# Kernel optimization log

Hardware: AMD Instinct MI355X
Metric: run time of the kernel (lower is better)

Reference implementation:

```python
import jax, jax.numpy as jnp
import numpy as np

B, S, D = 1, 2048, 2048
HQ, HKV, DH = 16, 4, 128
WINDOW = 512  # sliding window encoded in explicit attn_mask


def rotate_half(u):
    u1, u2 = jnp.split(u, 2, axis=-1)
    return jnp.concatenate([-u2, u1], axis=-1)


def setup_inputs() -> dict:
    key = jax.random.key(0)
    ks = jax.random.split(key, 6)
    x = jax.random.normal(ks[0], (B, S, D), dtype=jnp.float32)
    # RoPE caches (standard rotary frequencies, full d_head with duplicated halves)
    pos = jnp.arange(S)
    inv_freq = 1.0 / (10000.0 ** (jnp.arange(0, DH, 2, dtype=jnp.float32) / DH))
    ang = pos[:, None].astype(jnp.float32) * inv_freq[None, :]  # [S, DH/2]
    emb = jnp.concatenate([ang, ang], axis=-1)                  # [S, DH]
    cos_cache = jnp.cos(emb)
    sin_cache = jnp.sin(emb)
    # sliding-window causal mask: attend to j<=i and i-j < WINDOW
    i = jnp.arange(S)[:, None]
    j = jnp.arange(S)[None, :]
    attn_mask = (j <= i) & ((i - j) < WINDOW)
    sc = 0.02
    Wq = jax.random.normal(ks[1], (D, HQ * DH), dtype=jnp.float32) * sc
    Wk = jax.random.normal(ks[2], (D, HKV * DH), dtype=jnp.float32) * sc
    Wv = jax.random.normal(ks[3], (D, HKV * DH), dtype=jnp.float32) * sc
    Wo = jax.random.normal(ks[4], (HQ * DH, D), dtype=jnp.float32) * sc
    return {"x": x, "cos_cache": cos_cache, "sin_cache": sin_cache,
            "positions": pos.astype(jnp.int64), "attn_mask": attn_mask,
            "Wq": Wq, "Wk": Wk, "Wv": Wv, "Wo": Wo}


def reference(x, cos_cache, sin_cache, positions, attn_mask, Wq, Wk, Wv, Wo):
    batch, seq_len, _ = x.shape
    Q = (x @ Wq).reshape(batch, seq_len, HQ, DH).transpose(0, 2, 1, 3)   # [B,HQ,S,DH]
    K = (x @ Wk).reshape(batch, seq_len, HKV, DH).transpose(0, 2, 1, 3)  # [B,HKV,S,DH]
    V = (x @ Wv).reshape(batch, seq_len, HKV, DH).transpose(0, 2, 1, 3)
    # RoPE
    cos = cos_cache[positions][None, None, :, :]  # [1,1,S,DH]
    sin = sin_cache[positions][None, None, :, :]
    Q = Q * cos + rotate_half(Q) * sin
    K = K * cos + rotate_half(K) * sin
    # GQA expansion (repeat_interleave along head dim)
    G = HQ // HKV
    K_exp = jnp.repeat(K, G, axis=1)  # [B,HQ,S,DH]
    V_exp = jnp.repeat(V, G, axis=1)
    scores = jnp.einsum('bhqd,bhkd->bhqk', Q, K_exp) / jnp.sqrt(jnp.float32(DH))
    neg_inf = jnp.finfo(scores.dtype).min
    scores = jnp.where(attn_mask[None, None, :, :], scores, neg_inf)
    weights = jax.nn.softmax(scores, axis=-1)
    attn_out = jnp.einsum('bhqk,bhkd->bhqd', weights, V_exp)
    attn_out = attn_out.transpose(0, 2, 1, 3).reshape(batch, seq_len, HQ * DH)
    output = attn_out @ Wo
    return (output, K, V)  # new kv cache is the (post-RoPE) K, V
```

## Files before the change

### kernel.cpp

```cpp
#include <hip/hip_runtime.h>
#include <stdint.h>

typedef unsigned short u16;
typedef __attribute__((ext_vector_type(4))) float f32x4;
typedef __attribute__((ext_vector_type(8))) short short8;
typedef __attribute__((ext_vector_type(4))) short short4v;

__device__ inline u16 f2bf(float f) {
  union { float f; uint32_t u; } v; v.f = f;
  uint32_t u = v.u;
  u += 0x7fffu + ((u >> 16) & 1u);
  return (u16)(u >> 16);
}
__device__ inline float bf2f(u16 b) {
  union { uint32_t u; float f; } v; v.u = (uint32_t)b << 16; return v.f;
}

__global__ __launch_bounds__(256) void k_prep(const float* __restrict__ x,
                                              const float* __restrict__ Wq, const float* __restrict__ Wk,
                                              const float* __restrict__ Wv, const float* __restrict__ Wo,
                                              u16* __restrict__ xb, u16* __restrict__ WT, u16* __restrict__ WoT) {
  const int b = blockIdx.x, tid = threadIdx.x;
  if (b < 1024) {
    size_t base = (size_t)b * 4096 + tid * 4;
    #pragma unroll
    for (int k = 0; k < 4; ++k) {
      f32x4 v = *(const f32x4*)(x + base + k * 1024);
      short4v o;
      o.x = (short)f2bf(v.x); o.y = (short)f2bf(v.y);
      o.z = (short)f2bf(v.z); o.w = (short)f2bf(v.w);
      *(short4v*)(xb + base + k * 1024) = o;
    }
    return;
  }
  __shared__ float t[64][68];
  const float* W; u16* D; int N, bb;
  if (b < 2048)      { W = Wq; D = WT;                       N = 2048; bb = b - 1024; }
  else if (b < 2304) { W = Wk; D = WT + (size_t)2048 * 2048; N = 512;  bb = b - 2048; }
  else if (b < 2560) { W = Wv; D = WT + (size_t)2560 * 2048; N = 512;  bb = b - 2304; }
  else               { W = Wo; D = WoT;                      N = 2048; bb = b - 2560; }
  const int nb = N >> 6;
  const int n0 = (bb % nb) * 64, k0 = (bb / nb) * 64;
  const int c4 = (tid & 15) * 4, rbase = tid >> 4;
  #pragma unroll
  for (int p = 0; p < 4; ++p) {
    int r = p * 16 + rbase;
    *(f32x4*)&t[r][c4] = *(const f32x4*)&W[(size_t)(k0 + r) * N + n0 + c4];
  }
  __syncthreads();
  const int i = tid >> 2, j = (tid & 3) * 16;
  short8 o0, o1;
  #pragma unroll
  for (int m = 0; m < 8; ++m) o0[m] = (short)f2bf(t[j + m][i]);
  #pragma unroll
  for (int m = 0; m < 8; ++m) o1[m] = (short)f2bf(t[j + 8 + m][i]);
  *(short8*)&D[(size_t)(n0 + i) * 2048 + k0 + j] = o0;
  *(short8*)&D[(size_t)(n0 + i) * 2048 + k0 + j + 8] = o1;
}

__global__ __launch_bounds__(512, 2) void k_gemmqkv(const u16* __restrict__ A,
                                                    const u16* __restrict__ B,
                                                    u16* __restrict__ C) {
  const int K = 2048;
  const int NT = 32;
  __shared__ __align__(16) u16 lds[3 * 20480];
  const int tid = threadIdx.x;
  const int wid = tid >> 6, lane = tid & 63;
  const int quad = lane >> 4, l16 = lane & 15;
  const int wm = (wid >> 2) * 64;
  const int wn = (wid & 3) * 48;
  const int bm = blockIdx.y * 128, bn = blockIdx.x * 192;

  const u16* aSrc[2]; int aDst[2];
  #pragma unroll
  for (int L = 0; L < 2; ++L) {
    int E = (tid + L * 512) * 8;
    int r = E >> 6, pc = (E >> 3) & 7;
    int lc = pc ^ (r & 7);
    aSrc[L] = A + (size_t)(bm + r) * K + lc * 8;
    aDst[L] = E;
  }
  const u16* bSrc[3]; int bDst[3];
  #pragma unroll
  for (int L = 0; L < 3; ++L) {
    int E = (tid + L * 512) * 8;
    int r = E >> 6, pc = (E >> 3) & 7;
    int lc = pc ^ (r & 7);
    bSrc[L] = B + (size_t)(bn + r) * K + lc * 8;
    bDst[L] = 8192 + E;
  }

  #define STAGE(buf, kt) do {                                                              \
    _Pragma("unroll")                                                                      \
    for (int L = 0; L < 2; ++L)                                                            \
      __builtin_amdgcn_global_load_lds(                                                    \
          (const __attribute__((address_space(1))) void*)(aSrc[L] + (kt) * 64),            \
          (__attribute__((address_space(3))) void*)(&lds[(buf) * 20480 + aDst[L]]), 16, 0, 0); \
    _Pragma("unroll")                                                                      \
    for (int L = 0; L < 3; ++L)                                                            \
      __builtin_amdgcn_global_load_lds(                                                    \
          (const __attribute__((address_space(1))) void*)(bSrc[L] + (kt) * 64),            \
          (__attribute__((address_space(3))) void*)(&lds[(buf) * 20480 + bDst[L]]), 16, 0, 0); \
  } while (0)

  f32x4 acc[4][3];
  #pragma unroll
  for (int m = 0; m < 4; ++m)
    #pragma unroll
    for (int n = 0; n < 3; ++n) acc[m][n] = (f32x4){0.f, 0.f, 0.f, 0.f};

  STAGE(0, 0);
  STAGE(1, 1);
  asm volatile("s_waitcnt vmcnt(5)" ::: "memory");
  __builtin_amdgcn_s_barrier();

  int c = 0, p = 2;
  for (int t = 0; t < NT; ++t) {
    if (t + 2 < NT) STAGE(p, t + 2);

    short8 af[4][2], bf[3][2];
    #pragma unroll
    for (int mf = 0; mf < 4; ++mf)
      #pragma unroll
      for (int kc = 0; kc < 2; ++kc) {
        int R = wm + mf * 16 + l16;
        int pc = (kc * 4 + quad) ^ (R & 7);
        af[mf][kc] = *(const short8*)&lds[c * 20480 + R * 64 + pc * 8];
      }
    #pragma unroll
    for (int nf = 0; nf < 3; ++nf)
      #pragma unroll
      for (int kc = 0; kc < 2; ++kc) {
        int Cc = wn + nf * 16 + l16;
        int pc = (kc * 4 + quad) ^ (Cc & 7);
        bf[nf][kc] = *(const short8*)&lds[c * 20480 + 8192 + Cc * 64 + pc * 8];
      }

    __builtin_amdgcn_s_setprio(1);
    #pragma unroll
    for (int mf = 0; mf < 4; ++mf)
      #pragma unroll
      for (int nf = 0; nf < 3; ++nf)
        #pragma unroll
        for (int kc = 0; kc < 2; ++kc)
          acc[mf][nf] = __builtin_amdgcn_mfma_f32_16x16x32_bf16(af[mf][kc], bf[nf][kc], acc[mf][nf], 0, 0, 0);
    __builtin_amdgcn_s_setprio(0);

    if (t + 2 < NT) {
      asm volatile("s_waitcnt vmcnt(5)" ::: "memory");
    } else if (t + 1 < NT) {
      asm volatile("s_waitcnt vmcnt(0)" ::: "memory");
    }
    __builtin_amdgcn_s_barrier();
    c = (c == 2) ? 0 : c + 1;
    p = (p == 2) ? 0 : p + 1;
  }
  #undef STAGE

  #pragma unroll
  for (int mf = 0; mf < 4; ++mf) {
    int row = bm + wm + mf * 16 + quad * 4;
    #pragma unroll
    for (int nf = 0; nf < 3; ++nf) {
      int col = bn + wn + nf * 16 + l16;
      #pragma unroll
      for (int r = 0; r < 4; ++r)
        C[(size_t)(row + r) * 3072 + col] = f2bf(acc[mf][nf][r]);
    }
  }
}

__global__ __launch_bounds__(512, 2) void k_gemmo(const u16* __restrict__ A,
                                                  const u16* __restrict__ B,
                                                  float* __restrict__ C) {
  const int K = 2048;
  const int NT = 32;
  __shared__ __align__(16) u16 lds[3 * 16384];
  const int tid = threadIdx.x;
  const int wid = tid >> 6, lane = tid & 63;
  const int quad = lane >> 4, l16 = lane & 15;
  const int wm = (wid >> 2) * 64;
  const int wn = (wid & 3) * 32;
  const int bm = blockIdx.y * 128, bn = blockIdx.x * 128;

  const u16* aSrc[2]; const u16* bSrc[2]; int dDst[2];
  #pragma unroll
  for (int L = 0; L < 2; ++L) {
    int E = (tid + L * 512) * 8;
    int r = E >> 6, pc = (E >> 3) & 7;
    int lc = pc ^ (r & 7);
    aSrc[L] = A + (size_t)(bm + r) * K + lc * 8;
    bSrc[L] = B + (size_t)(bn + r) * K + lc * 8;
    dDst[L] = E;
  }

  #define STAGEO(buf, kt) do {                                                             \
    _Pragma("unroll")                                                                      \
    for (int L = 0; L < 2; ++L)                                                            \
      __builtin_amdgcn_global_load_lds(                                                    \
          (const __attribute__((address_space(1))) void*)(aSrc[L] + (kt) * 64),            \
          (__attribute__((address_space(3))) void*)(&lds[(buf) * 16384 + dDst[L]]), 16, 0, 0); \
    _Pragma("unroll")                                                                      \
    for (int L = 0; L < 2; ++L)                                                            \
      __builtin_amdgcn_global_load_lds(                                                    \
          (const __attribute__((address_space(1))) void*)(bSrc[L] + (kt) * 64),            \
          (__attribute__((address_space(3))) void*)(&lds[(buf) * 16384 + 8192 + dDst[L]]), 16, 0, 0); \
  } while (0)

  f32x4 acc[4][2];
  #pragma unroll
  for (int m = 0; m < 4; ++m)
    #pragma unroll
    for (int n = 0; n < 2; ++n) acc[m][n] = (f32x4){0.f, 0.f, 0.f, 0.f};

  STAGEO(0, 0);
  STAGEO(1, 1);
  asm volatile("s_waitcnt vmcnt(4)" ::: "memory");
  __builtin_amdgcn_s_barrier();

  int c = 0, p = 2;
  for (int t = 0; t < NT; ++t) {
    if (t + 2 < NT) STAGEO(p, t + 2);

    short8 af[4][2], bf[2][2];
    #pragma unroll
    for (int mf = 0; mf < 4; ++mf)
      #pragma unroll
      for (int kc = 0; kc < 2; ++kc) {
        int R = wm + mf * 16 + l16;
        int pc = (kc * 4 + quad) ^ (R & 7);
        af[mf][kc] = *(const short8*)&lds[c * 16384 + R * 64 + pc * 8];
      }
    #pragma unroll
    for (int nf = 0; nf < 2; ++nf)
      #pragma unroll
      for (int kc = 0; kc < 2; ++kc) {
        int Cc = wn + nf * 16 + l16;
        int pc = (kc * 4 + quad) ^ (Cc & 7);
        bf[nf][kc] = *(const short8*)&lds[c * 16384 + 8192 + Cc * 64 + pc * 8];
      }

    __builtin_amdgcn_s_setprio(1);
    #pragma unroll
    for (int mf = 0; mf < 4; ++mf)
      #pragma unroll
      for (int nf = 0; nf < 2; ++nf)
        #pragma unroll
        for (int kc = 0; kc < 2; ++kc)
          acc[mf][nf] = __builtin_amdgcn_mfma_f32_16x16x32_bf16(af[mf][kc], bf[nf][kc], acc[mf][nf], 0, 0, 0);
    __builtin_amdgcn_s_setprio(0);

    if (t + 2 < NT) {
      asm volatile("s_waitcnt vmcnt(4)" ::: "memory");
    } else if (t + 1 < NT) {
      asm volatile("s_waitcnt vmcnt(0)" ::: "memory");
    }
    __builtin_amdgcn_s_barrier();
    c = (c == 2) ? 0 : c + 1;
    p = (p == 2) ? 0 : p + 1;
  }
  #undef STAGEO

  #pragma unroll
  for (int mf = 0; mf < 4; ++mf) {
    int row = bm + wm + mf * 16 + quad * 4;
    #pragma unroll
    for (int nf = 0; nf < 2; ++nf) {
      int col = bn + wn + nf * 16 + l16;
      #pragma unroll
      for (int r = 0; r < 4; ++r)
        C[(size_t)(row + r) * 2048 + col] = acc[mf][nf][r];
    }
  }
}

__global__ __launch_bounds__(256) void k_post(const u16* __restrict__ P,
                                              const float* __restrict__ cosc, const float* __restrict__ sinc,
                                              u16* __restrict__ Qb, u16* __restrict__ Kb, u16* __restrict__ Vt,
                                              float* __restrict__ Kout, float* __restrict__ Vout) {
  const int b = blockIdx.x, tid = threadIdx.x;
  if (b < 2048) {
    __shared__ float row[3072];
    const int s = b;
    const u16* p0 = P + (size_t)s * 3072;
    for (int i = tid * 4; i < 3072; i += 1024) {
      short4v a0 = *(const short4v*)(p0 + i);
      #pragma unroll
      for (int m = 0; m < 4; ++m)
        row[i + m] = bf2f((u16)a0[m]);
    }
    __syncthreads();
    const int d = tid & 127;
    const int hbase = tid >> 7;
    const float c = cosc[s * 128 + d], sn = sinc[s * 128 + d];
    const float scale = 0.08838834764831845f;
    #pragma unroll
    for (int it = 0; it < 12; ++it) {
      int slice = it * 2 + hbase;
      float v = row[slice * 128 + d];
      if (slice < 20) {
        float other = (d < 64) ? -row[slice * 128 + d + 64] : row[slice * 128 + d - 64];
        float r = v * c + other * sn;
        if (slice < 16) {
          Qb[((size_t)slice * 2048 + s) * 128 + d] = f2bf(r * scale);
        } else {
          int hk = slice - 16;
          Kout[((size_t)hk * 2048 + s) * 128 + d] = r;
          Kb[((size_t)hk * 2048 + s) * 128 + d] = f2bf(r);
        }
      } else {
        int hv = slice - 20;
        Vout[((size_t)hv * 2048 + s) * 128 + d] = v;
      }
    }
  } else {
    __shared__ float t[32][33];
    const int b2 = b - 2048;
    const int c0 = (b2 & 15) * 32, s0 = (b2 >> 4) * 32;
    const int tx = tid & 31, ty = tid >> 5;
    #pragma unroll
    for (int i = ty; i < 32; i += 8) {
      size_t idx = (size_t)(s0 + i) * 3072 + 2560 + c0 + tx;
      t[i][tx] = bf2f(P[idx]);
    }
    __syncthreads();
    const int head = c0 >> 7, dbase = c0 & 127;
    #pragma unroll
    for (int i = ty; i < 32; i += 8)
      Vt[((size_t)head * 128 + dbase + i) * 2048 + s0 + tx] = f2bf(t[tx][i]);
  }
}

__global__ __launch_bounds__(512) void k_attn(const u16* __restrict__ Qb,
                                              const u16* __restrict__ Kb,
                                              const u16* __restrict__ Vt,
                                              u16* __restrict__ O) {
  const int qt = blockIdx.x;
  const int hk = blockIdx.y;
  const int tid = threadIdx.x;
  const int wid = tid >> 6, lane = tid & 63;
  const int quad = lane >> 4, l16 = lane & 15;
  const int h = hk * 4 + (wid >> 1);
  const int qrow0 = qt * 32;
  const int r0 = qrow0 + (wid & 1) * 16;
  const u16* Qh = Qb + (size_t)h * 2048 * 128;
  const u16* Kh = Kb + (size_t)hk * 2048 * 128;
  const u16* Vh = Vt + (size_t)hk * 128 * 2048;

  __shared__ u16 Ks[3][32 * 136];
  __shared__ u16 Vs[3][128 * 40];
  __shared__ u16 Ps[8][16 * 40];

  short8 qa[4];
  #pragma unroll
  for (int ks = 0; ks < 4; ++ks)
    qa[ks] = *(const short8*)&Qh[(size_t)(r0 + l16) * 128 + ks * 32 + quad * 8];

  f32x4 o[8];
  #pragma unroll
  for (int dt = 0; dt < 8; ++dt) o[dt] = (f32x4){0.f, 0.f, 0.f, 0.f};
  float lsum[4] = {0.f, 0.f, 0.f, 0.f};

  const int c0 = qrow0 > 511 ? (qrow0 - 511) >> 5 : 0;
  const int c1 = (qrow0 + 31) >> 5;

  const int krow = tid >> 4, kcol = (tid & 15) * 8;
  const int vrow = tid >> 2, vcol = (tid & 3) * 8;

  short8 kreg, vreg;
  {
    const int jb = c0 * 32;
    kreg = *(const short8*)&Kh[(size_t)(jb + krow) * 128 + kcol];
    vreg = *(const short8*)&Vh[(size_t)vrow * 2048 + jb + vcol];
  }

  for (int c = c0; c <= c1; ++c) {
    const int b = c % 3;
    const int jbase = c * 32;
    *(short8*)&Ks[b][krow * 136 + kcol] = kreg;
    *(short8*)&Vs[b][vrow * 40 + vcol] = vreg;
    if (c < c1) {
      const int jb = jbase + 32;
      kreg = *(const short8*)&Kh[(size_t)(jb + krow) * 128 + kcol];
      vreg = *(const short8*)&Vh[(size_t)vrow * 2048 + jb + vcol];
    }
    __syncthreads();

    f32x4 sc[2];
    #pragma unroll
    for (int ni = 0; ni < 2; ++ni) {
      sc[ni] = (f32x4){0.f, 0.f, 0.f, 0.f};
      #pragma unroll
      for (int ks = 0; ks < 4; ++ks) {
        short8 kf = *(const short8*)&Ks[b][(ni * 16 + l16) * 136 + ks * 32 + quad * 8];
        sc[ni] = __builtin_amdgcn_mfma_f32_16x16x32_bf16(qa[ks], kf, sc[ni], 0, 0, 0);
      }
    }
    #pragma unroll
    for (int ni = 0; ni < 2; ++ni) {
      const int jlo = jbase + ni * 16;
      const bool none = (jlo > r0 + 15) || (jlo + 15 < r0 - 511);
      const bool allv = (jlo + 15 <= r0) && (jlo >= r0 - 496);
      float p[4];
      if (none) {
        p[0] = p[1] = p[2] = p[3] = 0.f;
      } else if (allv) {
        #pragma unroll
        for (int r = 0; r < 4; ++r) p[r] = __expf(sc[ni][r]);
      } else {
        const int j = jlo + l16;
        #pragma unroll
        for (int r = 0; r < 4; ++r) {
          int i = r0 + quad * 4 + r;
          bool ok = (j <= i) && (i - j < 512);
          p[r] = ok ? __expf(sc[ni][r]) : 0.f;
        }
      }
      #pragma unroll
      for (int r = 0; r < 4; ++r) {
        lsum[r] += p[r];
        Ps[wid][(quad * 4 + r) * 40 + ni * 16 + l16] = f2bf(p[r]);
      }
    }
    short8 pa = *(const short8*)&Ps[wid][l16 * 40 + quad * 8];
    #pragma unroll
    for (int dt = 0; dt < 8; ++dt) {
      short8 vf = *(const short8*)&Vs[b][(dt * 16 + l16) * 40 + quad * 8];
      o[dt] = __builtin_amdgcn_mfma_f32_16x16x32_bf16(pa, vf, o[dt], 0, 0, 0);
    }
  }

  #pragma unroll
  for (int off = 1; off < 16; off <<= 1)
    #pragma unroll
    for (int r = 0; r < 4; ++r)
      lsum[r] += __shfl_xor(lsum[r], off, 64);
  float inv[4];
  #pragma unroll
  for (int r = 0; r < 4; ++r) inv[r] = 1.0f / lsum[r];

  #pragma unroll
  for (int dt = 0; dt < 8; ++dt) {
    int col = h * 128 + dt * 16 + l16;
    #pragma unroll
    for (int r = 0; r < 4; ++r) {
      int row = r0 + quad * 4 + r;
      O[(size_t)row * 2048 + col] = f2bf(o[dt][r] * inv[r]);
    }
  }
}

extern "C" void kernel_launch(void* const* d_in, const int* in_sizes, int n_in,
                              void* d_out, int out_size, void* d_ws, size_t ws_size,
                              hipStream_t stream) {
  const float* x    = (const float*)d_in[0];
  const float* cosc = (const float*)d_in[1];
  const float* sinc = (const float*)d_in[2];
  const float* Wq = (const float*)d_in[5];
  const float* Wk = (const float*)d_in[6];
  const float* Wv = (const float*)d_in[7];
  const float* Wo = (const float*)d_in[8];

  char* ws = (char*)d_ws;
  u16*   xb    = (u16*)(ws);
  u16*   O     = (u16*)(ws);
  u16*   WT    = (u16*)(ws + (8u  << 20));
  u16*   WoT   = (u16*)(ws + (20u << 20));
  u16*   Qb    = (u16*)(ws + (28u << 20));
  u16*   Kb    = (u16*)(ws + (36u << 20));
  u16*   Vt    = (u16*)(ws + (38u << 20));
  u16*   QKV   = (u16*)(ws + (40u << 20));

  float* outO = (float*)d_out;
  float* outK = (float*)d_out + 4194304;
  float* outV = (float*)d_out + 5242880;

  k_prep<<<3584, 256, 0, stream>>>(x, Wq, Wk, Wv, Wo, xb, WT, WoT);
  k_gemmqkv<<<dim3(16, 16), 512, 0, stream>>>(xb, WT, QKV);
  k_post<<<3072, 256, 0, stream>>>(QKV, cosc, sinc, Qb, Kb, Vt, outK, outV);
  k_attn<<<dim3(64, 4), 512, 0, stream>>>(Qb, Kb, Vt, O);
  k_gemmo<<<dim3(16, 16), 512, 0, stream>>>(O, WoT, outO);
}
```

Measured before the change: 101.6 us.

## Fuse RoPE and Q/K scatter into QKV GEMM epilogue via permuted weight columns

The weight-prep kernel now permutes Wq/Wk output columns so each rotate-half pair (d, d+64) sits in adjacent columns. The QKV GEMM epilogue can then apply RoPE with a lane shuffle and write Qb, Kb and the fp32 K output directly. The post kernel shrinks to a V-only transpose that also writes the fp32 V output. This removes the full bf16 QKV round trip through global memory and most of the post kernel. The cost is scattered, uncoalesced epilogue stores plus per-element cos/sin loads inside the GEMM. It also relies on the permuted Q/K head-dim layout in Qb/Kb being harmless, which holds only because attention takes a dot product over the head dimension.

Result: slower. 107.5 us (+5.8%).

```diff
diff --git a/kernel.cpp b/kernel.cpp
--- a/kernel.cpp
+++ b/kernel.cpp
@@ -34,33 +34,45 @@
     return;
   }
   __shared__ float t[64][68];
-  const float* W; u16* D; int N, bb;
-  if (b < 2048)      { W = Wq; D = WT;                       N = 2048; bb = b - 1024; }
-  else if (b < 2304) { W = Wk; D = WT + (size_t)2048 * 2048; N = 512;  bb = b - 2048; }
-  else if (b < 2560) { W = Wv; D = WT + (size_t)2560 * 2048; N = 512;  bb = b - 2304; }
-  else               { W = Wo; D = WoT;                      N = 2048; bb = b - 2560; }
+  const float* W; u16* D; int N, bb; bool perm;
+  if (b < 2048)      { W = Wq; D = WT;                       N = 2048; bb = b - 1024; perm = true;  }
+  else if (b < 2304) { W = Wk; D = WT + (size_t)2048 * 2048; N = 512;  bb = b - 2048; perm = true;  }
+  else if (b < 2560) { W = Wv; D = WT + (size_t)2560 * 2048; N = 512;  bb = b - 2304; perm = false; }
+  else               { W = Wo; D = WoT;                      N = 2048; bb = b - 2560; perm = false; }
   const int nb = N >> 6;
   const int n0 = (bb % nb) * 64, k0 = (bb / nb) * 64;
   const int c4 = (tid & 15) * 4, rbase = tid >> 4;
+  int scol;
+  if (perm) {
+    int S0 = (n0 & ~127) + ((n0 >> 6) & 1) * 32;
+    scol = (c4 < 32) ? (S0 + c4) : (S0 + 64 + (c4 - 32));
+  } else {
+    scol = n0 + c4;
+  }
   #pragma unroll
   for (int p = 0; p < 4; ++p) {
     int r = p * 16 + rbase;
-    *(f32x4*)&t[r][c4] = *(const f32x4*)&W[(size_t)(k0 + r) * N + n0 + c4];
+    *(f32x4*)&t[r][c4] = *(const f32x4*)&W[(size_t)(k0 + r) * N + scol];
   }
   __syncthreads();
   const int i = tid >> 2, j = (tid & 3) * 16;
+  const int tcol = perm ? ((i >> 1) + 32 * (i & 1)) : i;
   short8 o0, o1;
   #pragma unroll
-  for (int m = 0; m < 8; ++m) o0[m] = (short)f2bf(t[j + m][i]);
-  #pragma unroll
-  for (int m = 0; m < 8; ++m) o1[m] = (short)f2bf(t[j + 8 + m][i]);
+  for (int m = 0; m < 8; ++m) o0[m] = (short)f2bf(t[j + m][tcol]);
+  #pragma unroll
+  for (int m = 0; m < 8; ++m) o1[m] = (short)f2bf(t[j + 8 + m][tcol]);
   *(short8*)&D[(size_t)(n0 + i) * 2048 + k0 + j] = o0;
   *(short8*)&D[(size_t)(n0 + i) * 2048 + k0 + j + 8] = o1;
 }
 
 __global__ __launch_bounds__(512, 2) void k_gemmqkv(const u16* __restrict__ A,
                                                     const u16* __restrict__ B,
-                                                    u16* __restrict__ C) {
+                                                    const float* __restrict__ cosc,
+                                                    const float* __restrict__ sinc,
+                                                    u16* __restrict__ Qb, u16* __restrict__ Kb,
+                                                    float* __restrict__ Kout,
+                                                    u16* __restrict__ Vraw) {
   const int K = 2048;
   const int NT = 32;
   __shared__ __align__(16) u16 lds[3 * 20480];
@@ -157,15 +169,39 @@
   }
   #undef STAGE
 
+  const float scale = 0.08838834764831845f;
   #pragma unroll
   for (int mf = 0; mf < 4; ++mf) {
-    int row = bm + wm + mf * 16 + quad * 4;
+    int srow = bm + wm + mf * 16 + quad * 4;
     #pragma unroll
     for (int nf = 0; nf < 3; ++nf) {
-      int col = bn + wn + nf * 16 + l16;
-      #pragma unroll
-      for (int r = 0; r < 4; ++r)
-        C[(size_t)(row + r) * 3072 + col] = f2bf(acc[mf][nf][r]);
+      int cb = bn + wn + nf * 16;
+      if (cb >= 2560) {
+        #pragma unroll
+        for (int r = 0; r < 4; ++r)
+          Vraw[(size_t)(srow + r) * 512 + (cb - 2560) + l16] = f2bf(acc[mf][nf][r]);
+      } else {
+        const int tcol = (cb & 127) + l16;
+        const int pp = tcol >> 1;
+        const int odd = l16 & 1;
+        #pragma unroll
+        for (int r = 0; r < 4; ++r) {
+          float v = acc[mf][nf][r];
+          float w = __shfl_xor(v, 1, 64);
+          int s = srow + r;
+          float cc = cosc[s * 128 + pp];
+          float ss = sinc[s * 128 + pp];
+          float res = odd ? (v * cc + w * ss) : (v * cc - w * ss);
+          if (cb < 2048) {
+            int h = cb >> 7;
+            Qb[((size_t)h * 2048 + s) * 128 + tcol] = f2bf(res * scale);
+          } else {
+            int hk = (cb - 2048) >> 7;
+            Kb[((size_t)hk * 2048 + s) * 128 + tcol] = f2bf(res);
+            Kout[((size_t)hk * 2048 + s) * 128 + pp + 64 * odd] = res;
+          }
+        }
+      }
     }
   }
 }
@@ -274,60 +310,22 @@
   }
 }
 
-__global__ __launch_bounds__(256) void k_post(const u16* __restrict__ P,
-                                              const float* __restrict__ cosc, const float* __restrict__ sinc,
-                                              u16* __restrict__ Qb, u16* __restrict__ Kb, u16* __restrict__ Vt,
-                                              float* __restrict__ Kout, float* __restrict__ Vout) {
-  const int b = blockIdx.x, tid = threadIdx.x;
-  if (b < 2048) {
-    __shared__ float row[3072];
-    const int s = b;
-    const u16* p0 = P + (size_t)s * 3072;
-    for (int i = tid * 4; i < 3072; i += 1024) {
-      short4v a0 = *(const short4v*)(p0 + i);
-      #pragma unroll
-      for (int m = 0; m < 4; ++m)
-        row[i + m] = bf2f((u16)a0[m]);
-    }
-    __syncthreads();
-    const int d = tid & 127;
-    const int hbase = tid >> 7;
-    const float c = cosc[s * 128 + d], sn = sinc[s * 128 + d];
-    const float scale = 0.08838834764831845f;
-    #pragma unroll
-    for (int it = 0; it < 12; ++it) {
-      int slice = it * 2 + hbase;
-      float v = row[slice * 128 + d];
-      if (slice < 20) {
-        float other = (d < 64) ? -row[slice * 128 + d + 64] : row[slice * 128 + d - 64];
-        float r = v * c + other * sn;
-        if (slice < 16) {
-          Qb[((size_t)slice * 2048 + s) * 128 + d] = f2bf(r * scale);
-        } else {
-          int hk = slice - 16;
-          Kout[((size_t)hk * 2048 + s) * 128 + d] = r;
-          Kb[((size_t)hk * 2048 + s) * 128 + d] = f2bf(r);
-        }
-      } else {
-        int hv = slice - 20;
-        Vout[((size_t)hv * 2048 + s) * 128 + d] = v;
-      }
-    }
-  } else {
-    __shared__ float t[32][33];
-    const int b2 = b - 2048;
-    const int c0 = (b2 & 15) * 32, s0 = (b2 >> 4) * 32;
-    const int tx = tid & 31, ty = tid >> 5;
-    #pragma unroll
-    for (int i = ty; i < 32; i += 8) {
-      size_t idx = (size_t)(s0 + i) * 3072 + 2560 + c0 + tx;
-      t[i][tx] = bf2f(P[idx]);
-    }
-    __syncthreads();
-    const int head = c0 >> 7, dbase = c0 & 127;
-    #pragma unroll
-    for (int i = ty; i < 32; i += 8)
-      Vt[((size_t)head * 128 + dbase + i) * 2048 + s0 + tx] = f2bf(t[tx][i]);
+__global__ __launch_bounds__(256) void k_post(const u16* __restrict__ Vraw,
+                                              u16* __restrict__ Vt, float* __restrict__ Vout) {
+  __shared__ float t[32][33];
+  const int b2 = blockIdx.x;
+  const int c0 = (b2 & 15) * 32, s0 = (b2 >> 4) * 32;
+  const int tid = threadIdx.x;
+  const int tx = tid & 31, ty = tid >> 5;
+  #pragma unroll
+  for (int i = ty; i < 32; i += 8)
+    t[i][tx] = bf2f(Vraw[(size_t)(s0 + i) * 512 + c0 + tx]);
+  __syncthreads();
+  const int head = c0 >> 7, dbase = c0 & 127;
+  #pragma unroll
+  for (int i = ty; i < 32; i += 8) {
+    Vt[((size_t)head * 128 + dbase + i) * 2048 + s0 + tx] = f2bf(t[tx][i]);
+    Vout[((size_t)head * 2048 + s0 + i) * 128 + dbase + tx] = t[i][tx];
   }
 }
 
@@ -469,15 +467,15 @@
   u16*   Qb    = (u16*)(ws + (28u << 20));
   u16*   Kb    = (u16*)(ws + (36u << 20));
   u16*   Vt    = (u16*)(ws + (38u << 20));
-  u16*   QKV   = (u16*)(ws + (40u << 20));
+  u16*   Vraw  = (u16*)(ws + (40u << 20));
 
   float* outO = (float*)d_out;
   float* outK = (float*)d_out + 4194304;
   float* outV = (float*)d_out + 5242880;
 
   k_prep<<<3584, 256, 0, stream>>>(x, Wq, Wk, Wv, Wo, xb, WT, WoT);
-  k_gemmqkv<<<dim3(16, 16), 512, 0, stream>>>(xb, WT, QKV);
-  k_post<<<3072, 256, 0, stream>>>(QKV, cosc, sinc, Qb, Kb, Vt, outK, outV);
+  k_gemmqkv<<<dim3(16, 16), 512, 0, stream>>>(xb, WT, cosc, sinc, Qb, Kb, outK, Vraw);
+  k_post<<<1024, 256, 0, stream>>>(Vraw, Vt, outV);
   k_attn<<<dim3(64, 4), 512, 0, stream>>>(Qb, Kb, Vt, O);
   k_gemmo<<<dim3(16, 16), 512, 0, stream>>>(O, WoT, outO);
 }
```

## Double GEMM block threads to 1024 and split A/B tile loading across waves

Applied to the files above, without the earlier changes.

Both projection GEMMs now launch 1024-thread blocks (16 waves), with each wave computing a 32-row slice instead of 64 rows of the same 128-row block tile. Global-to-LDS staging is split so the first 512 threads load the A tile and the rest load the B tile, and the per-thread vmcnt waits are adjusted to match. The intent is more waves per CU to hide memory and MFMA latency while keeping the grid unchanged. The cost is that each fragment read from LDS is reused across fewer MFMAs, and the launch-bounds setting tightens register limits.

Measured after the change: 104.0 us. 1.02x slower.

```diff
diff --git a/kernel.cpp b/kernel.cpp
--- a/kernel.cpp
+++ b/kernel.cpp
@@ -58,69 +58,65 @@
   *(short8*)&D[(size_t)(n0 + i) * 2048 + k0 + j + 8] = o1;
 }
 
-__global__ __launch_bounds__(512, 2) void k_gemmqkv(const u16* __restrict__ A,
-                                                    const u16* __restrict__ B,
-                                                    u16* __restrict__ C) {
+__global__ __launch_bounds__(1024, 4) void k_gemmqkv(const u16* __restrict__ A,
+                                                     const u16* __restrict__ B,
+                                                     u16* __restrict__ C) {
   const int K = 2048;
   const int NT = 32;
   __shared__ __align__(16) u16 lds[3 * 20480];
   const int tid = threadIdx.x;
   const int wid = tid >> 6, lane = tid & 63;
   const int quad = lane >> 4, l16 = lane & 15;
-  const int wm = (wid >> 2) * 64;
+  const int wm = (wid >> 2) * 32;
   const int wn = (wid & 3) * 48;
   const int bm = blockIdx.y * 128, bn = blockIdx.x * 192;
 
-  const u16* aSrc[2]; int aDst[2];
-  #pragma unroll
-  for (int L = 0; L < 2; ++L) {
-    int E = (tid + L * 512) * 8;
+  const bool isA = tid < 512;
+  const int ts = isA ? tid : tid - 512;
+  const u16* src[3]; int dst[3];
+  #pragma unroll
+  for (int L = 0; L < 3; ++L) {
+    int s = ts + L * 512;
+    if (isA && L == 2) s = ts;
+    int E = s * 8;
     int r = E >> 6, pc = (E >> 3) & 7;
     int lc = pc ^ (r & 7);
-    aSrc[L] = A + (size_t)(bm + r) * K + lc * 8;
-    aDst[L] = E;
-  }
-  const u16* bSrc[3]; int bDst[3];
-  #pragma unroll
-  for (int L = 0; L < 3; ++L) {
-    int E = (tid + L * 512) * 8;
-    int r = E >> 6, pc = (E >> 3) & 7;
-    int lc = pc ^ (r & 7);
-    bSrc[L] = B + (size_t)(bn + r) * K + lc * 8;
-    bDst[L] = 8192 + E;
+    if (isA) { src[L] = A + (size_t)(bm + r) * K + lc * 8; dst[L] = E; }
+    else     { src[L] = B + (size_t)(bn + r) * K + lc * 8; dst[L] = 8192 + E; }
   }
 
   #define STAGE(buf, kt) do {                                                              \
-    _Pragma("unroll")                                                                      \
-    for (int L = 0; L < 2; ++L)                                                            \
+    __builtin_amdgcn_global_load_lds(                                                      \
+        (const __attribute__((address_space(1))) void*)(src[0] + (kt) * 64),               \
+        (__attribute__((address_space(3))) void*)(&lds[(buf) * 20480 + dst[0]]), 16, 0, 0);\
+    __builtin_amdgcn_global_load_lds(                                                      \
+        (const __attribute__((address_space(1))) void*)(src[1] + (kt) * 64),               \
+        (__attribute__((address_space(3))) void*)(&lds[(buf) * 20480 + dst[1]]), 16, 0, 0);\
+    if (!isA)                                                                              \
       __builtin_amdgcn_global_load_lds(                                                    \
-          (const __attribute__((address_space(1))) void*)(aSrc[L] + (kt) * 64),            \
-          (__attribute__((address_space(3))) void*)(&lds[(buf) * 20480 + aDst[L]]), 16, 0, 0); \
-    _Pragma("unroll")                                                                      \
-    for (int L = 0; L < 3; ++L)                                                            \
-      __builtin_amdgcn_global_load_lds(                                                    \
-          (const __attribute__((address_space(1))) void*)(bSrc[L] + (kt) * 64),            \
-          (__attribute__((address_space(3))) void*)(&lds[(buf) * 20480 + bDst[L]]), 16, 0, 0); \
+          (const __attribute__((address_space(1))) void*)(src[2] + (kt) * 64),             \
+          (__attribute__((address_space(3))) void*)(&lds[(buf) * 20480 + dst[2]]), 16, 0, 0);\
   } while (0)
 
-  f32x4 acc[4][3];
-  #pragma unroll
-  for (int m = 0; m < 4; ++m)
+  f32x4 acc[2][3];
+  #pragma unroll
+  for (int m = 0; m < 2; ++m)
     #pragma unroll
     for (int n = 0; n < 3; ++n) acc[m][n] = (f32x4){0.f, 0.f, 0.f, 0.f};
 
   STAGE(0, 0);
   STAGE(1, 1);
-  asm volatile("s_waitcnt vmcnt(5)" ::: "memory");
+  if (isA) { asm volatile("s_waitcnt vmcnt(2)" ::: "memory"); }
+  else     { asm volatile("s_waitcnt vmcnt(3)" ::: "memory"); }
   __builtin_amdgcn_s_barrier();
 
   int c = 0, p = 2;
   for (int t = 0; t < NT; ++t) {
     if (t + 2 < NT) STAGE(p, t + 2);
 
-    short8 af[4][2], bf[3][2];
-    #pragma unroll
-    for (int mf = 0; mf < 4; ++mf)
+    short8 af[2][2], bf[3][2];
+    #pragma unroll
+    for (int mf = 0; mf < 2; ++mf)
       #pragma unroll
       for (int kc = 0; kc < 2; ++kc) {
         int R = wm + mf * 16 + l16;
@@ -138,7 +134,7 @@
 
     __builtin_amdgcn_s_setprio(1);
     #pragma unroll
-    for (int mf = 0; mf < 4; ++mf)
+    for (int mf = 0; mf < 2; ++mf)
       #pragma unroll
       for (int nf = 0; nf < 3; ++nf)
         #pragma unroll
@@ -147,7 +143,8 @@
     __builtin_amdgcn_s_setprio(0);
 
     if (t + 2 < NT) {
-      asm volatile("s_waitcnt vmcnt(5)" ::: "memory");
+      if (isA) { asm volatile("s_waitcnt vmcnt(2)" ::: "memory"); }
+      else     { asm volatile("s_waitcnt vmcnt(3)" ::: "memory"); }
     } else if (t + 1 < NT) {
       asm volatile("s_waitcnt vmcnt(0)" ::: "memory");
     }
@@ -158,7 +155,7 @@
   #undef STAGE
 
   #pragma unroll
-  for (int mf = 0; mf < 4; ++mf) {
+  for (int mf = 0; mf < 2; ++mf) {
     int row = bm + wm + mf * 16 + quad * 4;
     #pragma unroll
     for (int nf = 0; nf < 3; ++nf) {
@@ -170,61 +167,57 @@
   }
 }
 
-__global__ __launch_bounds__(512, 2) void k_gemmo(const u16* __restrict__ A,
-                                                  const u16* __restrict__ B,
-                                                  float* __restrict__ C) {
+__global__ __launch_bounds__(1024, 4) void k_gemmo(const u16* __restrict__ A,
+                                                   const u16* __restrict__ B,
+                                                   float* __restrict__ C) {
   const int K = 2048;
   const int NT = 32;
   __shared__ __align__(16) u16 lds[3 * 16384];
   const int tid = threadIdx.x;
   const int wid = tid >> 6, lane = tid & 63;
   const int quad = lane >> 4, l16 = lane & 15;
-  const int wm = (wid >> 2) * 64;
+  const int wm = (wid >> 2) * 32;
   const int wn = (wid & 3) * 32;
   const int bm = blockIdx.y * 128, bn = blockIdx.x * 128;
 
-  const u16* aSrc[2]; const u16* bSrc[2]; int dDst[2];
+  const bool isA = tid < 512;
+  const int ts = isA ? tid : tid - 512;
+  const u16* src[2]; int dst[2];
   #pragma unroll
   for (int L = 0; L < 2; ++L) {
-    int E = (tid + L * 512) * 8;
+    int E = (ts + L * 512) * 8;
     int r = E >> 6, pc = (E >> 3) & 7;
     int lc = pc ^ (r & 7);
-    aSrc[L] = A + (size_t)(bm + r) * K + lc * 8;
-    bSrc[L] = B + (size_t)(bn + r) * K + lc * 8;
-    dDst[L] = E;
+    if (isA) { src[L] = A + (size_t)(bm + r) * K + lc * 8; dst[L] = E; }
+    else     { src[L] = B + (size_t)(bn + r) * K + lc * 8; dst[L] = 8192 + E; }
   }
 
   #define STAGEO(buf, kt) do {                                                             \
     _Pragma("unroll")                                                                      \
     for (int L = 0; L < 2; ++L)                                                            \
       __builtin_amdgcn_global_load_lds(                                                    \
-          (const __attribute__((address_space(1))) void*)(aSrc[L] + (kt) * 64),            \
-          (__attribute__((address_space(3))) void*)(&lds[(buf) * 16384 + dDst[L]]), 16, 0, 0); \
-    _Pragma("unroll")                                                                      \
-    for (int L = 0; L < 2; ++L)                                                            \
-      __builtin_amdgcn_global_load_lds(                                                    \
-          (const __attribute__((address_space(1))) void*)(bSrc[L] + (kt) * 64),            \
-          (__attribute__((address_space(3))) void*)(&lds[(buf) * 16384 + 8192 + dDst[L]]), 16, 0, 0); \
+          (const __attribute__((address_space(1))) void*)(src[L] + (kt) * 64),             \
+          (__attribute__((address_space(3))) void*)(&lds[(buf) * 16384 + dst[L]]), 16, 0, 0); \
   } while (0)
 
-  f32x4 acc[4][2];
-  #pragma unroll
-  for (int m = 0; m < 4; ++m)
+  f32x4 acc[2][2];
+  #pragma unroll
+  for (int m = 0; m < 2; ++m)
     #pragma unroll
     for (int n = 0; n < 2; ++n) acc[m][n] = (f32x4){0.f, 0.f, 0.f, 0.f};
 
   STAGEO(0, 0);
   STAGEO(1, 1);
-  asm volatile("s_waitcnt vmcnt(4)" ::: "memory");
+  asm volatile("s_waitcnt vmcnt(2)" ::: "memory");
   __builtin_amdgcn_s_barrier();
 
   int c = 0, p = 2;
   for (int t = 0; t < NT; ++t) {
     if (t + 2 < NT) STAGEO(p, t + 2);
 
-    short8 af[4][2], bf[2][2];
-    #pragma unroll
-    for (int mf = 0; mf < 4; ++mf)
+    short8 af[2][2], bf[2][2];
+    #pragma unroll
+    for (int mf = 0; mf < 2; ++mf)
       #pragma unroll
       for (int kc = 0; kc < 2; ++kc) {
         int R = wm + mf * 16 + l16;
@@ -242,7 +235,7 @@
 
     __builtin_amdgcn_s_setprio(1);
     #pragma unroll
-    for (int mf = 0; mf < 4; ++mf)
+    for (int mf = 0; mf < 2; ++mf)
       #pragma unroll
       for (int nf = 0; nf < 2; ++nf)
         #pragma unroll
@@ -251,7 +244,7 @@
     __builtin_amdgcn_s_setprio(0);
 
     if (t + 2 < NT) {
-      asm volatile("s_waitcnt vmcnt(4)" ::: "memory");
+      asm volatile("s_waitcnt vmcnt(2)" ::: "memory");
     } else if (t + 1 < NT) {
       asm volatile("s_waitcnt vmcnt(0)" ::: "memory");
     }
@@ -262,7 +255,7 @@
   #undef STAGEO
 
   #pragma unroll
-  for (int mf = 0; mf < 4; ++mf) {
+  for (int mf = 0; mf < 2; ++mf) {
     int row = bm + wm + mf * 16 + quad * 4;
     #pragma unroll
     for (int nf = 0; nf < 2; ++nf) {
@@ -476,8 +469,8 @@
   float* outV = (float*)d_out + 5242880;
 
   k_prep<<<3584, 256, 0, stream>>>(x, Wq, Wk, Wv, Wo, xb, WT, WoT);
-  k_gemmqkv<<<dim3(16, 16), 512, 0, stream>>>(xb, WT, QKV);
+  k_gemmqkv<<<dim3(16, 16), 1024, 0, stream>>>(xb, WT, QKV);
   k_post<<<3072, 256, 0, stream>>>(QKV, cosc, sinc, Qb, Kb, Vt, outK, outV);
   k_attn<<<dim3(64, 4), 512, 0, stream>>>(Qb, Kb, Vt, O);
-  k_gemmo<<<dim3(16, 16), 512, 0, stream>>>(O, WoT, outO);
-}
+  k_gemmo<<<dim3(16, 16), 1024, 0, stream>>>(O, WoT, outO);
+}
```

## Use smaller 256-thread GEMM tiles with simple double buffering

Applied to the files above, without the earlier changes.

Both GEMM kernels move from 512-thread blocks with 128x192/128x128 tiles and a 3-stage async pipeline to 256-thread blocks with 128x96/128x64 tiles and a 2-stage double buffer synchronized by __syncthreads. The grids double to 512 blocks, aiming for better CU coverage and balance. In exchange, per-block data reuse drops and global-load latency is less hidden, since each barrier waits for all outstanding loads. The setprio hints are also removed.

Result: slower. 106.2 us (+4.5%).

```diff
diff --git a/kernel.cpp b/kernel.cpp
--- a/kernel.cpp
+++ b/kernel.cpp
@@ -58,23 +58,23 @@
   *(short8*)&D[(size_t)(n0 + i) * 2048 + k0 + j + 8] = o1;
 }
 
-__global__ __launch_bounds__(512, 2) void k_gemmqkv(const u16* __restrict__ A,
-                                                    const u16* __restrict__ B,
-                                                    u16* __restrict__ C) {
+__global__ __launch_bounds__(256) void k_gemmqkv(const u16* __restrict__ A,
+                                                 const u16* __restrict__ B,
+                                                 u16* __restrict__ C) {
   const int K = 2048;
   const int NT = 32;
-  __shared__ __align__(16) u16 lds[3 * 20480];
+  __shared__ __align__(16) u16 lds[2 * 14336];
   const int tid = threadIdx.x;
   const int wid = tid >> 6, lane = tid & 63;
   const int quad = lane >> 4, l16 = lane & 15;
-  const int wm = (wid >> 2) * 64;
-  const int wn = (wid & 3) * 48;
-  const int bm = blockIdx.y * 128, bn = blockIdx.x * 192;
-
-  const u16* aSrc[2]; int aDst[2];
-  #pragma unroll
-  for (int L = 0; L < 2; ++L) {
-    int E = (tid + L * 512) * 8;
+  const int wm = (wid >> 1) * 64;
+  const int wn = (wid & 1) * 48;
+  const int bm = blockIdx.y * 128, bn = blockIdx.x * 96;
+
+  const u16* aSrc[4]; int aDst[4];
+  #pragma unroll
+  for (int L = 0; L < 4; ++L) {
+    int E = (tid + L * 256) * 8;
     int r = E >> 6, pc = (E >> 3) & 7;
     int lc = pc ^ (r & 7);
     aSrc[L] = A + (size_t)(bm + r) * K + lc * 8;
@@ -83,7 +83,7 @@
   const u16* bSrc[3]; int bDst[3];
   #pragma unroll
   for (int L = 0; L < 3; ++L) {
-    int E = (tid + L * 512) * 8;
+    int E = (tid + L * 256) * 8;
     int r = E >> 6, pc = (E >> 3) & 7;
     int lc = pc ^ (r & 7);
     bSrc[L] = B + (size_t)(bn + r) * K + lc * 8;
@@ -92,15 +92,15 @@
 
   #define STAGE(buf, kt) do {                                                              \
     _Pragma("unroll")                                                                      \
-    for (int L = 0; L < 2; ++L)                                                            \
+    for (int L = 0; L < 4; ++L)                                                            \
       __builtin_amdgcn_global_load_lds(                                                    \
           (const __attribute__((address_space(1))) void*)(aSrc[L] + (kt) * 64),            \
-          (__attribute__((address_space(3))) void*)(&lds[(buf) * 20480 + aDst[L]]), 16, 0, 0); \
+          (__attribute__((address_space(3))) void*)(&lds[(buf) * 14336 + aDst[L]]), 16, 0, 0); \
     _Pragma("unroll")                                                                      \
     for (int L = 0; L < 3; ++L)                                                            \
       __builtin_amdgcn_global_load_lds(                                                    \
           (const __attribute__((address_space(1))) void*)(bSrc[L] + (kt) * 64),            \
-          (__attribute__((address_space(3))) void*)(&lds[(buf) * 20480 + bDst[L]]), 16, 0, 0); \
+          (__attribute__((address_space(3))) void*)(&lds[(buf) * 14336 + bDst[L]]), 16, 0, 0); \
   } while (0)
 
   f32x4 acc[4][3];
@@ -110,13 +110,11 @@
     for (int n = 0; n < 3; ++n) acc[m][n] = (f32x4){0.f, 0.f, 0.f, 0.f};
 
   STAGE(0, 0);
-  STAGE(1, 1);
-  asm volatile("s_waitcnt vmcnt(5)" ::: "memory");
-  __builtin_amdgcn_s_barrier();
-
-  int c = 0, p = 2;
+  __syncthreads();
+
   for (int t = 0; t < NT; ++t) {
-    if (t + 2 < NT) STAGE(p, t + 2);
+    const int c = t & 1;
+    if (t + 1 < NT) STAGE(c ^ 1, t + 1);
 
     short8 af[4][2], bf[3][2];
     #pragma unroll
@@ -125,7 +123,7 @@
       for (int kc = 0; kc < 2; ++kc) {
         int R = wm + mf * 16 + l16;
         int pc = (kc * 4 + quad) ^ (R & 7);
-        af[mf][kc] = *(const short8*)&lds[c * 20480 + R * 64 + pc * 8];
+        af[mf][kc] = *(const short8*)&lds[c * 14336 + R * 64 + pc * 8];
       }
     #pragma unroll
     for (int nf = 0; nf < 3; ++nf)
@@ -133,10 +131,9 @@
       for (int kc = 0; kc < 2; ++kc) {
         int Cc = wn + nf * 16 + l16;
         int pc = (kc * 4 + quad) ^ (Cc & 7);
-        bf[nf][kc] = *(const short8*)&lds[c * 20480 + 8192 + Cc * 64 + pc * 8];
-      }
-
-    __builtin_amdgcn_s_setprio(1);
+        bf[nf][kc] = *(const short8*)&lds[c * 14336 + 8192 + Cc * 64 + pc * 8];
+      }
+
     #pragma unroll
     for (int mf = 0; mf < 4; ++mf)
       #pragma unroll
@@ -144,16 +141,8 @@
         #pragma unroll
         for (int kc = 0; kc < 2; ++kc)
           acc[mf][nf] = __builtin_amdgcn_mfma_f32_16x16x32_bf16(af[mf][kc], bf[nf][kc], acc[mf][nf], 0, 0, 0);
-    __builtin_amdgcn_s_setprio(0);
-
-    if (t + 2 < NT) {
-      asm volatile("s_waitcnt vmcnt(5)" ::: "memory");
-    } else if (t + 1 < NT) {
-      asm volatile("s_waitcnt vmcnt(0)" ::: "memory");
-    }
-    __builtin_amdgcn_s_barrier();
-    c = (c == 2) ? 0 : c + 1;
-    p = (p == 2) ? 0 : p + 1;
+
+    __syncthreads();
   }
   #undef STAGE
 
@@ -170,41 +159,49 @@
   }
 }
 
-__global__ __launch_bounds__(512, 2) void k_gemmo(const u16* __restrict__ A,
-                                                  const u16* __restrict__ B,
-                                                  float* __restrict__ C) {
+__global__ __launch_bounds__(256) void k_gemmo(const u16* __restrict__ A,
+                                               const u16* __restrict__ B,
+                                               float* __restrict__ C) {
   const int K = 2048;
   const int NT = 32;
-  __shared__ __align__(16) u16 lds[3 * 16384];
+  __shared__ __align__(16) u16 lds[2 * 12288];
   const int tid = threadIdx.x;
   const int wid = tid >> 6, lane = tid & 63;
   const int quad = lane >> 4, l16 = lane & 15;
-  const int wm = (wid >> 2) * 64;
-  const int wn = (wid & 3) * 32;
-  const int bm = blockIdx.y * 128, bn = blockIdx.x * 128;
-
-  const u16* aSrc[2]; const u16* bSrc[2]; int dDst[2];
-  #pragma unroll
-  for (int L = 0; L < 2; ++L) {
-    int E = (tid + L * 512) * 8;
+  const int wm = (wid >> 1) * 64;
+  const int wn = (wid & 1) * 32;
+  const int bm = blockIdx.y * 128, bn = blockIdx.x * 64;
+
+  const u16* aSrc[4]; int aDst[4];
+  #pragma unroll
+  for (int L = 0; L < 4; ++L) {
+    int E = (tid + L * 256) * 8;
     int r = E >> 6, pc = (E >> 3) & 7;
     int lc = pc ^ (r & 7);
     aSrc[L] = A + (size_t)(bm + r) * K + lc * 8;
+    aDst[L] = E;
+  }
+  const u16* bSrc[2]; int bDst[2];
+  #pragma unroll
+  for (int L = 0; L < 2; ++L) {
+    int E = (tid + L * 256) * 8;
+    int r = E >> 6, pc = (E >> 3) & 7;
+    int lc = pc ^ (r & 7);
     bSrc[L] = B + (size_t)(bn + r) * K + lc * 8;
-    dDst[L] = E;
+    bDst[L] = 8192 + E;
   }
 
   #define STAGEO(buf, kt) do {                                                             \
     _Pragma("unroll")                                                                      \
-    for (int L = 0; L < 2; ++L)                                                            \
+    for (int L = 0; L < 4; ++L)                                                            \
       __builtin_amdgcn_global_load_lds(                                                    \
           (const __attribute__((address_space(1))) void*)(aSrc[L] + (kt) * 64),            \
-          (__attribute__((address_space(3))) void*)(&lds[(buf) * 16384 + dDst[L]]), 16, 0, 0); \
+          (__attribute__((address_space(3))) void*)(&lds[(buf) * 12288 + aDst[L]]), 16, 0, 0); \
     _Pragma("unroll")                                                                      \
     for (int L = 0; L < 2; ++L)                                                            \
       __builtin_amdgcn_global_load_lds(                                                    \
           (const __attribute__((address_space(1))) void*)(bSrc[L] + (kt) * 64),            \
-          (__attribute__((address_space(3))) void*)(&lds[(buf) * 16384 + 8192 + dDst[L]]), 16, 0, 0); \
+          (__attribute__((address_space(3))) void*)(&lds[(buf) * 12288 + bDst[L]]), 16, 0, 0); \
   } while (0)
 
   f32x4 acc[4][2];
@@ -214,13 +211,11 @@
     for (int n = 0; n < 2; ++n) acc[m][n] = (f32x4){0.f, 0.f, 0.f, 0.f};
 
   STAGEO(0, 0);
-  STAGEO(1, 1);
-  asm volatile("s_waitcnt vmcnt(4)" ::: "memory");
-  __builtin_amdgcn_s_barrier();
-
-  int c = 0, p = 2;
+  __syncthreads();
+
   for (int t = 0; t < NT; ++t) {
-    if (t + 2 < NT) STAGEO(p, t + 2);
+    const int c = t & 1;
+    if (t + 1 < NT) STAGEO(c ^ 1, t + 1);
 
     short8 af[4][2], bf[2][2];
     #pragma unroll
@@ -229,7 +224,7 @@
       for (int kc = 0; kc < 2; ++kc) {
         int R = wm + mf * 16 + l16;
         int pc = (kc * 4 + quad) ^ (R & 7);
-        af[mf][kc] = *(const short8*)&lds[c * 16384 + R * 64 + pc * 8];
+        af[mf][kc] = *(const short8*)&lds[c * 12288 + R * 64 + pc * 8];
       }
     #pragma unroll
     for (int nf = 0; nf < 2; ++nf)
@@ -237,10 +232,9 @@
       for (int kc = 0; kc < 2; ++kc) {
         int Cc = wn + nf * 16 + l16;
         int pc = (kc * 4 + quad) ^ (Cc & 7);
-        bf[nf][kc] = *(const short8*)&lds[c * 16384 + 8192 + Cc * 64 + pc * 8];
-      }
-
-    __builtin_amdgcn_s_setprio(1);
+        bf[nf][kc] = *(const short8*)&lds[c * 12288 + 8192 + Cc * 64 + pc * 8];
+      }
+
     #pragma unroll
     for (int mf = 0; mf < 4; ++mf)
       #pragma unroll
@@ -248,16 +242,8 @@
         #pragma unroll
         for (int kc = 0; kc < 2; ++kc)
           acc[mf][nf] = __builtin_amdgcn_mfma_f32_16x16x32_bf16(af[mf][kc], bf[nf][kc], acc[mf][nf], 0, 0, 0);
-    __builtin_amdgcn_s_setprio(0);
-
-    if (t + 2 < NT) {
-      asm volatile("s_waitcnt vmcnt(4)" ::: "memory");
-    } else if (t + 1 < NT) {
-      asm volatile("s_waitcnt vmcnt(0)" ::: "memory");
-    }
-    __builtin_amdgcn_s_barrier();
-    c = (c == 2) ? 0 : c + 1;
-    p = (p == 2) ? 0 : p + 1;
+
+    __syncthreads();
   }
   #undef STAGEO
 
@@ -476,8 +462,8 @@
   float* outV = (float*)d_out + 5242880;
 
   k_prep<<<3584, 256, 0, stream>>>(x, Wq, Wk, Wv, Wo, xb, WT, WoT);
-  k_gemmqkv<<<dim3(16, 16), 512, 0, stream>>>(xb, WT, QKV);
+  k_gemmqkv<<<dim3(32, 16), 256, 0, stream>>>(xb, WT, QKV);
   k_post<<<3072, 256, 0, stream>>>(QKV, cosc, sinc, Qb, Kb, Vt, outK, outV);
   k_attn<<<dim3(64, 4), 512, 0, stream>>>(Qb, Kb, Vt, O);
-  k_gemmo<<<dim3(16, 16), 512, 0, stream>>>(O, WoT, outO);
-}
+  k_gemmo<<<dim3(32, 16), 256, 0, stream>>>(O, WoT, outO);
+}
```
